# Optimization experiments

Hardware: AMD Instinct MI355X
Metric: run time of the kernel (lower is better)

The kernel has to match this reference:

```python
import jax, jax.numpy as jnp
import numpy as np
from jax import lax

V, D, H, L, NH, OUT = 30000, 300, 512, 2, 8, 3
HD = 2 * H // NH  # 128
B, S = 32, 512


def setup_inputs() -> dict:
    key = jax.random.key(0)
    ks = iter(jax.random.split(key, 64))
    def p(*shape):
        return jax.random.normal(next(ks), shape, jnp.float32) * 0.02
    inp = {"x": jax.random.randint(next(ks), (B, S), 0, V)}
    inp["emb"] = p(V, D)
    for l in range(L):
        isz = D if l == 0 else 2 * H
        for d in ("f", "b"):
            inp[f"Wih_{l}{d}"] = p(4 * H, isz)
            inp[f"Whh_{l}{d}"] = p(4 * H, H)
            inp[f"bih_{l}{d}"] = p(4 * H)
            inp[f"bhh_{l}{d}"] = p(4 * H)
    inp["Wq"], inp["bq"] = p(NH, 2 * H, HD), p(NH, HD)
    inp["Wk"], inp["bk"] = p(NH, 2 * H, HD), p(NH, HD)
    inp["Wv"], inp["bv"] = p(NH, 2 * H, HD), p(NH, HD)
    inp["Wfc"], inp["bfc"] = p(OUT, 2 * H), p(OUT)
    return inp


def _lstm_dir(x, Wih, Whh, bih, bhh, reverse):
    # x: [B,S,I]; PyTorch gate order i,f,g,o
    xg = jnp.einsum('bsi,gi->sbg', x, Wih) + bih  # precomputed input projections [S,B,4H]
    Bn = x.shape[0]
    init = (jnp.zeros((Bn, H), x.dtype), jnp.zeros((Bn, H), x.dtype))
    def step(carry, xt):
        h, c = carry
        g = xt + h @ Whh.T + bhh
        i, f, gg, o = jnp.split(g, 4, axis=-1)
        c = jax.nn.sigmoid(f) * c + jax.nn.sigmoid(i) * jnp.tanh(gg)
        h = jax.nn.sigmoid(o) * jnp.tanh(c)
        return (h, c), h
    _, hs = lax.scan(step, init, xg, reverse=reverse)
    return jnp.swapaxes(hs, 0, 1)  # [B,S,H]


def _forward(x, emb, lstm_params, Wq, bq, Wk, bk, Wv, bv, Wfc, bfc):
    h = emb[x]  # [B,S,D]
    for (Wf, Uf, bf1, bf2, Wb, Ub, bb1, bb2) in lstm_params:
        fwd = _lstm_dir(h, Wf, Uf, bf1, bf2, reverse=False)
        bwd = _lstm_dir(h, Wb, Ub, bb1, bb2, reverse=True)
        h = jnp.concatenate([fwd, bwd], axis=-1)  # [B,S,2H]
    # multi-head attention over LSTM outputs (heads batched instead of python loop)
    Q = jnp.einsum('bsd,hde->bhse', h, Wq) + bq[None, :, None, :]
    K = jnp.einsum('bsd,hde->bhse', h, Wk) + bk[None, :, None, :]
    Vv = jnp.einsum('bsd,hde->bhse', h, Wv) + bv[None, :, None, :]
    scores = jax.nn.softmax(jnp.einsum('bhse,bhte->bhst', Q, K) / np.sqrt(HD).astype(np.float32), axis=-1)
    ctx = jnp.einsum('bhst,bhte->bhse', scores, Vv)
    ctx = jnp.transpose(ctx, (0, 2, 1, 3)).reshape(ctx.shape[0], ctx.shape[2], NH * HD)  # concat heads
    pooled = jnp.mean(ctx, axis=1)  # [B,2H]
    return pooled @ Wfc.T + bfc


def reference(x, emb,
              Wih_0f, Whh_0f, bih_0f, bhh_0f, Wih_0b, Whh_0b, bih_0b, bhh_0b,
              Wih_1f, Whh_1f, bih_1f, bhh_1f, Wih_1b, Whh_1b, bih_1b, bhh_1b,
              Wq, bq, Wk, bk, Wv, bv, Wfc, bfc):
    lstm_params = [
        (Wih_0f, Whh_0f, bih_0f, bhh_0f, Wih_0b, Whh_0b, bih_0b, bhh_0b),
        (Wih_1f, Whh_1f, bih_1f, bhh_1f, Wih_1b, Whh_1b, bih_1b, bhh_1b),
    ]
    return _forward(x, emb, lstm_params, Wq, bq, Wk, bk, Wv, bv, Wfc, bfc)
```

## Files before the change

kernel.cpp:

```cpp
#include <hip/hip_runtime.h>
#include <hip/hip_bf16.h>
#include <math.h>

#define S_LEN 512
#define BATCH 32
#define HID   512
#define G4    2048
#define DIM   300
#define NHEAD 8
#define HDIM  128
#define CH    64
#define NCH   8

typedef __hip_bfloat16 bf16;

#define OFF_XGC   0ull
#define OFF_HCAT0 8388608ull
#define OFF_HCAT1 25165824ull
#define OFF_H0    25165824ull
#define OFF_WP    41943040ull
#define OFF_PB    45088768ull
#define OFF_CT    45091840ull
#define OFF_HT    45124608ull
#define OFF_POOL  45190144ull

__global__ void k_embed(const int* __restrict__ x, const float* __restrict__ emb,
                        float* __restrict__ h0)
{
    int p = blockIdx.x;
    int row = x[p];
    const float* src = emb + (size_t)row * DIM;
    float* dst = h0 + (size_t)p * DIM;
    for (int d = threadIdx.x; d < DIM; d += blockDim.x) dst[d] = src[d];
}

__global__ __launch_bounds__(256) void k_xgc(const float* __restrict__ A, int lda,
    const float* __restrict__ Wf, const float* __restrict__ Wb,
    const float* __restrict__ bihf, const float* __restrict__ bhhf,
    const float* __restrict__ bihb, const float* __restrict__ bhhb,
    float* __restrict__ xgc, int K, int c64)
{
    __shared__ float As[8][128];
    __shared__ float Bs[8][128];
    int tid = threadIdx.x;
    int dir = blockIdx.z;
    int m0 = blockIdx.y * 128, n0 = blockIdx.x * 128;
    const float* W  = dir ? Wb : Wf;
    const float* b1 = dir ? bihb : bihf;
    const float* b2 = dir ? bhhb : bhhf;
    int tx = tid & 15, ty = tid >> 4;

    float acc[8][8];
#pragma unroll
    for (int i = 0; i < 8; i++)
#pragma unroll
        for (int j = 0; j < 8; j++) acc[i][j] = 0.f;

    for (int k0 = 0; k0 < K; k0 += 8) {
#pragma unroll
        for (int e4 = 0; e4 < 4; e4++) {
            int e = tid * 4 + e4;
            int kl = e & 7, ml = e >> 3;
            int kk = k0 + kl;
            int m = m0 + ml;
            int slot = m >> 5, bb = m & 31;
            int s = dir ? (S_LEN - 1 - c64 - slot) : (c64 + slot);
            As[kl][ml] = (kk < K) ? A[((size_t)bb * S_LEN + s) * lda + kk] : 0.f;
            Bs[kl][ml] = (kk < K) ? W[(size_t)(n0 + ml) * K + kk] : 0.f;
        }
        __syncthreads();
#pragma unroll
        for (int k = 0; k < 8; k++) {
            float a[8], b[8];
#pragma unroll
            for (int i = 0; i < 8; i++) a[i] = As[k][ty + 16 * i];
#pragma unroll
            for (int j = 0; j < 8; j++) b[j] = Bs[k][tx + 16 * j];
#pragma unroll
            for (int i = 0; i < 8; i++)
#pragma unroll
                for (int j = 0; j < 8; j++) acc[i][j] += a[i] * b[j];
        }
        __syncthreads();
    }

#pragma unroll
    for (int i = 0; i < 8; i++) {
        int m = m0 + ty + 16 * i;
        int slot = m >> 5, bb = m & 31;
#pragma unroll
        for (int j = 0; j < 8; j++) {
            int n = n0 + tx + 16 * j;
            xgc[(((size_t)dir * CH + slot) * G4 + n) * BATCH + bb] =
                acc[i][j] + b1[n] + b2[n];
        }
    }
}

__global__ __launch_bounds__(256) void k_step(const float* __restrict__ xgc,
    const float* __restrict__ Whh_f, const float* __restrict__ Whh_b,
    float* __restrict__ hT, float* __restrict__ cT, float* __restrict__ hcat, int tt)
{
    int wg = blockIdx.x;
    int dir = wg >> 7, ublk = wg & 127;
    int u0 = ublk * 4;
    const float* Whh = dir ? Whh_b : Whh_f;
    int s_cur = dir ? (S_LEN - 1 - tt) : tt;
    int slot = tt & (CH - 1);
    int tid = threadIdx.x;
    int b  = tid & 31;
    int uu = (tid >> 5) & 3;
    int kh = tid >> 7;
    int u = u0 + uu;

    float acc0 = 0.f, acc1 = 0.f, acc2 = 0.f, acc3 = 0.f;
    if (tt > 0) {
        const float* hTd = hT + ((size_t)((tt & 1) ^ 1) * 2 + dir) * 16384;
        int k0 = kh * 256;
        const float4* w0 = (const float4*)(Whh + ((size_t)(0 * HID + u)) * HID + k0);
        const float4* w1 = (const float4*)(Whh + ((size_t)(1 * HID + u)) * HID + k0);
        const float4* w2 = (const float4*)(Whh + ((size_t)(2 * HID + u)) * HID + k0);
        const float4* w3 = (const float4*)(Whh + ((size_t)(3 * HID + u)) * HID + k0);
        const float* hb = hTd + (size_t)k0 * 32 + b;
#pragma unroll 8
        for (int k4 = 0; k4 < 64; k4++) {
            float h0v = hb[(k4 * 4 + 0) * 32];
            float h1v = hb[(k4 * 4 + 1) * 32];
            float h2v = hb[(k4 * 4 + 2) * 32];
            float h3v = hb[(k4 * 4 + 3) * 32];
            float4 a0 = w0[k4], a1 = w1[k4], a2 = w2[k4], a3 = w3[k4];
            acc0 += a0.x * h0v + a0.y * h1v + a0.z * h2v + a0.w * h3v;
            acc1 += a1.x * h0v + a1.y * h1v + a1.z * h2v + a1.w * h3v;
            acc2 += a2.x * h0v + a2.y * h1v + a2.z * h2v + a2.w * h3v;
            acc3 += a3.x * h0v + a3.y * h1v + a3.z * h2v + a3.w * h3v;
        }
    }

    __shared__ float red[4][4][32];
    if (kh) {
        red[uu][0][b] = acc0; red[uu][1][b] = acc1;
        red[uu][2][b] = acc2; red[uu][3][b] = acc3;
    }
    __syncthreads();
    if (!kh) {
        size_t xbase = (((size_t)dir * CH + slot) * G4) * BATCH;
        float gi = acc0 + red[uu][0][b] + xgc[xbase + (size_t)(0 * HID + u) * BATCH + b];
        float gf = acc1 + red[uu][1][b] + xgc[xbase + (size_t)(1 * HID + u) * BATCH + b];
        float gg = acc2 + red[uu][2][b] + xgc[xbase + (size_t)(2 * HID + u) * BATCH + b];
        float go = acc3 + red[uu][3][b] + xgc[xbase + (size_t)(3 * HID + u) * BATCH + b];
        size_t ci = ((size_t)dir * HID + u) * 32 + b;
        float cp = (tt > 0) ? cT[ci] : 0.f;
        float si = 1.f / (1.f + expf(-gi));
        float sf = 1.f / (1.f + expf(-gf));
        float so = 1.f / (1.f + expf(-go));
        float cn = sf * cp + si * tanhf(gg);
        float hn = so * tanhf(cn);
        cT[ci] = cn;
        hT[((size_t)(tt & 1) * 2 + dir) * 16384 + (size_t)u * 32 + b] = hn;
        hcat[((size_t)b * S_LEN + s_cur) * 1024 + dir * HID + u] = hn;
    }
}

__global__ void k_pack(const float* __restrict__ Wq, const float* __restrict__ Wk,
                       const float* __restrict__ Wv, const float* __restrict__ bq,
                       const float* __restrict__ bk, const float* __restrict__ bv,
                       float* __restrict__ Wp, float* __restrict__ pb)
{
    size_t i = (size_t)blockIdx.x * 256 + threadIdx.x;
    if (i < 3ull * 1024 * 1024) {
        int tt = (int)(i >> 20);
        int w  = (int)(i & 1048575);
        int n  = w >> 10;
        int d  = w & 1023;
        int hh = n >> 7, e = n & 127;
        const float* W = (tt == 0) ? Wq : (tt == 1 ? Wk : Wv);
        Wp[i] = W[((size_t)hh * 1024 + d) * 128 + e];
    }
    if (i < 3072) {
        int tt = (int)(i >> 10), w = (int)(i & 1023);
        const float* bb = (tt == 0) ? bq : (tt == 1 ? bk : bv);
        pb[i] = bb[w];
    }
}

__global__ __launch_bounds__(256) void k_qkv(const float* __restrict__ A,
    const float* __restrict__ Wp, const float* __restrict__ pb,
    bf16* __restrict__ Qout)
{
    __shared__ float As[8][128];
    __shared__ float Bs[8][128];
    int tid = threadIdx.x;
    int m0 = blockIdx.y * 128, n0 = blockIdx.x * 128;
    int tx = tid & 15, ty = tid >> 4;

    float acc[8][8];
#pragma unroll
    for (int i = 0; i < 8; i++)
#pragma unroll
        for (int j = 0; j < 8; j++) acc[i][j] = 0.f;

    for (int k0 = 0; k0 < 1024; k0 += 8) {
#pragma unroll
        for (int e4 = 0; e4 < 4; e4++) {
            int e = tid * 4 + e4;
            int kl = e & 7, ml = e >> 3;
            int kk = k0 + kl;
            As[kl][ml] = A[(size_t)(m0 + ml) * 1024 + kk];
            Bs[kl][ml] = Wp[(size_t)(n0 + ml) * 1024 + kk];
        }
        __syncthreads();
#pragma unroll
        for (int k = 0; k < 8; k++) {
            float a[8], b[8];
#pragma unroll
            for (int i = 0; i < 8; i++) a[i] = As[k][ty + 16 * i];
#pragma unroll
            for (int j = 0; j < 8; j++) b[j] = Bs[k][tx + 16 * j];
#pragma unroll
            for (int i = 0; i < 8; i++)
#pragma unroll
                for (int j = 0; j < 8; j++) acc[i][j] += a[i] * b[j];
        }
        __syncthreads();
    }

#pragma unroll
    for (int i = 0; i < 8; i++) {
        int m = m0 + ty + 16 * i;
        int b = m >> 9, s = m & 511;
#pragma unroll
        for (int j = 0; j < 8; j++) {
            int n = n0 + tx + 16 * j;
            int tt = n >> 10, w = n & 1023, hh = w >> 7, e = w & 127;
            float v = acc[i][j] + pb[n];
            Qout[(size_t)tt * 16777216ull +
                 ((size_t)(b * NHEAD + hh) * S_LEN + s) * HDIM + e] = __float2bfloat16(v);
        }
    }
}

__global__ __launch_bounds__(256) void k_attn(const bf16* __restrict__ Q,
    const bf16* __restrict__ K, const bf16* __restrict__ V,
    float* __restrict__ pooled)
{
    int bh = blockIdx.x;
    int b = bh >> 3, h = bh & 7;
    const bf16* Qb = Q + (size_t)bh * S_LEN * HDIM;
    const bf16* Kb = K + (size_t)bh * S_LEN * HDIM;
    const bf16* Vb = V + (size_t)bh * S_LEN * HDIM;

    __shared__ float Qs[16][HDIM];
    __shared__ float Ss[16][S_LEN + 4];
    __shared__ float wsum[S_LEN];

    int tid = threadIdx.x;
    for (int t = tid; t < S_LEN; t += 256) wsum[t] = 0.f;
    const float SC = 0.08838834764831845f;

    for (int rb = 0; rb < 32; rb++) {
        __syncthreads();
        for (int e = tid; e < 16 * HDIM; e += 256) {
            int rr = e >> 7, ee = e & 127;
            Qs[rr][ee] = __bfloat162float(Qb[(size_t)(rb * 16 + rr) * HDIM + ee]);
        }
        __syncthreads();
        float acc0[16], acc1[16];
#pragma unroll
        for (int r = 0; r < 16; r++) { acc0[r] = 0.f; acc1[r] = 0.f; }
        const bf16* k0p = Kb + (size_t)tid * HDIM;
        const bf16* k1p = Kb + (size_t)(tid + 256) * HDIM;
        for (int k = 0; k < HDIM; k += 4) {
            short4 r0 = *(const short4*)(k0p + k);
            short4 r1 = *(const short4*)(k1p + k);
            float k0x = __bfloat162float(*(const bf16*)&r0.x);
            float k0y = __bfloat162float(*(const bf16*)&r0.y);
            float k0z = __bfloat162float(*(const bf16*)&r0.z);
            float k0w = __bfloat162float(*(const bf16*)&r0.w);
            float k1x = __bfloat162float(*(const bf16*)&r1.x);
            float k1y = __bfloat162float(*(const bf16*)&r1.y);
            float k1z = __bfloat162float(*(const bf16*)&r1.z);
            float k1w = __bfloat162float(*(const bf16*)&r1.w);
#pragma unroll
            for (int r = 0; r < 16; r++) {
                float4 q = *(const float4*)&Qs[r][k];
                acc0[r] += q.x * k0x + q.y * k0y + q.z * k0z + q.w * k0w;
                acc1[r] += q.x * k1x + q.y * k1y + q.z * k1z + q.w * k1w;
            }
        }
#pragma unroll
        for (int r = 0; r < 16; r++) {
            Ss[r][tid] = acc0[r];
            Ss[r][tid + 256] = acc1[r];
        }
        __syncthreads();
        {
            int r = tid >> 4, l = tid & 15;
            float m = -1e30f;
            for (int t = l; t < S_LEN; t += 16) m = fmaxf(m, Ss[r][t]);
#pragma unroll
            for (int o = 1; o < 16; o <<= 1) m = fmaxf(m, __shfl_xor(m, o));
            float sum = 0.f;
            for (int t = l; t < S_LEN; t += 16) {
                float p = expf((Ss[r][t] - m) * SC);
                Ss[r][t] = p;
                sum += p;
            }
#pragma unroll
            for (int o = 1; o < 16; o <<= 1) sum += __shfl_xor(sum, o);
            float inv = 1.f / sum;
            for (int t = l; t < S_LEN; t += 16) Ss[r][t] *= inv;
        }
        __syncthreads();
        for (int t = tid; t < S_LEN; t += 256) {
            float s = 0.f;
#pragma unroll
            for (int rr = 0; rr < 16; rr++) s += Ss[rr][t];
            wsum[t] += s;
        }
    }
    __syncthreads();

    if (tid < HDIM) {
        float a = 0.f;
        for (int t = 0; t < S_LEN; t++)
            a += wsum[t] * __bfloat162float(Vb[(size_t)t * HDIM + tid]);
        pooled[(size_t)b * 1024 + h * HDIM + tid] = a * (1.0f / S_LEN);
    }
}

__global__ void k_fc(const float* __restrict__ pooled, const float* __restrict__ Wfc,
                     const float* __restrict__ bfc, float* __restrict__ out)
{
    int j = threadIdx.x;
    if (j < 96) {
        int b = j / 3, o = j - b * 3;
        float a = bfc[o];
        for (int k = 0; k < 1024; k++)
            a += pooled[(size_t)b * 1024 + k] * Wfc[(size_t)o * 1024 + k];
        out[j] = a;
    }
}

extern "C" void kernel_launch(void* const* d_in, const int* in_sizes, int n_in,
                              void* d_out, int out_size, void* d_ws, size_t ws_size,
                              hipStream_t stream)
{
    const int*   x     = (const int*)d_in[0];
    const float* emb   = (const float*)d_in[1];
    const float* Wih0f = (const float*)d_in[2];
    const float* Whh0f = (const float*)d_in[3];
    const float* bih0f = (const float*)d_in[4];
    const float* bhh0f = (const float*)d_in[5];
    const float* Wih0b = (const float*)d_in[6];
    const float* Whh0b = (const float*)d_in[7];
    const float* bih0b = (const float*)d_in[8];
    const float* bhh0b = (const float*)d_in[9];
    const float* Wih1f = (const float*)d_in[10];
    const float* Whh1f = (const float*)d_in[11];
    const float* bih1f = (const float*)d_in[12];
    const float* bhh1f = (const float*)d_in[13];
    const float* Wih1b = (const float*)d_in[14];
    const float* Whh1b = (const float*)d_in[15];
    const float* bih1b = (const float*)d_in[16];
    const float* bhh1b = (const float*)d_in[17];
    const float* Wq    = (const float*)d_in[18];
    const float* bq    = (const float*)d_in[19];
    const float* Wk    = (const float*)d_in[20];
    const float* bk    = (const float*)d_in[21];
    const float* Wv    = (const float*)d_in[22];
    const float* bv    = (const float*)d_in[23];
    const float* Wfc   = (const float*)d_in[24];
    const float* bfc   = (const float*)d_in[25];

    float* ws     = (float*)d_ws;
    float* xgc    = ws + OFF_XGC;
    float* hcat0  = ws + OFF_HCAT0;
    float* hcat1  = ws + OFF_HCAT1;
    float* h0     = ws + OFF_H0;
    float* Wp     = ws + OFF_WP;
    float* pb     = ws + OFF_PB;
    float* cT     = ws + OFF_CT;
    float* hT     = ws + OFF_HT;
    float* pooled = ws + OFF_POOL;
    bf16*  Qbf    = (bf16*)ws;
    bf16*  Kbf    = Qbf + 16777216ull;
    bf16*  Vbf    = Qbf + 33554432ull;

    dim3 blk(256);

    k_embed<<<BATCH * S_LEN, 128, 0, stream>>>(x, emb, h0);
    k_pack<<<12288, 256, 0, stream>>>(Wq, Wk, Wv, bq, bk, bv, Wp, pb);

    for (int c = 0; c < NCH; c++) {
        k_xgc<<<dim3(16, 16, 2), blk, 0, stream>>>(h0, DIM, Wih0f, Wih0b,
            bih0f, bhh0f, bih0b, bhh0b, xgc, DIM, c * CH);
        for (int i = 0; i < CH; i++)
            k_step<<<256, blk, 0, stream>>>(xgc, Whh0f, Whh0b, hT, cT, hcat0, c * CH + i);
    }
    for (int c = 0; c < NCH; c++) {
        k_xgc<<<dim3(16, 16, 2), blk, 0, stream>>>(hcat0, 1024, Wih1f, Wih1b,
            bih1f, bhh1f, bih1b, bhh1b, xgc, 1024, c * CH);
        for (int i = 0; i < CH; i++)
            k_step<<<256, blk, 0, stream>>>(xgc, Whh1f, Whh1b, hT, cT, hcat1, c * CH + i);
    }

    k_qkv<<<dim3(24, 128), blk, 0, stream>>>(hcat1, Wp, pb, Qbf);
    k_attn<<<256, blk, 0, stream>>>(Qbf, Kbf, Vbf, pooled);
    k_fc<<<1, 128, 0, stream>>>(pooled, Wfc, bfc, (float*)d_out);
}
```

Baseline: 24.19 ms.

## Replace per-timestep LSTM launches with persistent chunk kernel and grid barrier

```diff
diff --git a/kernel.cpp b/kernel.cpp
--- a/kernel.cpp
+++ b/kernel.cpp
@@ -21,8 +21,9 @@
 #define OFF_WP    41943040ull
 #define OFF_PB    45088768ull
 #define OFF_CT    45091840ull
-#define OFF_HT    45124608ull
+#define OFF_HG    45124608ull
 #define OFF_POOL  45190144ull
+#define OFF_BAR   45222912ull
 
 __global__ void k_embed(const int* __restrict__ x, const float* __restrict__ emb,
                         float* __restrict__ h0)
@@ -97,68 +98,119 @@
     }
 }
 
-__global__ __launch_bounds__(256) void k_step(const float* __restrict__ xgc,
+__global__ __launch_bounds__(512) void k_chunk(const float* __restrict__ xgc,
     const float* __restrict__ Whh_f, const float* __restrict__ Whh_b,
-    float* __restrict__ hT, float* __restrict__ cT, float* __restrict__ hcat, int tt)
-{
+    float* __restrict__ hG, float* __restrict__ cT, float* __restrict__ hcat,
+    unsigned int* __restrict__ bar, int c64)
+{
+    __shared__ float Wldsf[16 * 512];
     int wg = blockIdx.x;
     int dir = wg >> 7, ublk = wg & 127;
     int u0 = ublk * 4;
     const float* Whh = dir ? Whh_b : Whh_f;
-    int s_cur = dir ? (S_LEN - 1 - tt) : tt;
-    int slot = tt & (CH - 1);
     int tid = threadIdx.x;
-    int b  = tid & 31;
-    int uu = (tid >> 5) & 3;
-    int kh = tid >> 7;
-    int u = u0 + uu;
-
-    float acc0 = 0.f, acc1 = 0.f, acc2 = 0.f, acc3 = 0.f;
-    if (tt > 0) {
-        const float* hTd = hT + ((size_t)((tt & 1) ^ 1) * 2 + dir) * 16384;
-        int k0 = kh * 256;
-        const float4* w0 = (const float4*)(Whh + ((size_t)(0 * HID + u)) * HID + k0);
-        const float4* w1 = (const float4*)(Whh + ((size_t)(1 * HID + u)) * HID + k0);
-        const float4* w2 = (const float4*)(Whh + ((size_t)(2 * HID + u)) * HID + k0);
-        const float4* w3 = (const float4*)(Whh + ((size_t)(3 * HID + u)) * HID + k0);
-        const float* hb = hTd + (size_t)k0 * 32 + b;
-#pragma unroll 8
-        for (int k4 = 0; k4 < 64; k4++) {
-            float h0v = hb[(k4 * 4 + 0) * 32];
-            float h1v = hb[(k4 * 4 + 1) * 32];
-            float h2v = hb[(k4 * 4 + 2) * 32];
-            float h3v = hb[(k4 * 4 + 3) * 32];
-            float4 a0 = w0[k4], a1 = w1[k4], a2 = w2[k4], a3 = w3[k4];
-            acc0 += a0.x * h0v + a0.y * h1v + a0.z * h2v + a0.w * h3v;
-            acc1 += a1.x * h0v + a1.y * h1v + a1.z * h2v + a1.w * h3v;
-            acc2 += a2.x * h0v + a2.y * h1v + a2.z * h2v + a2.w * h3v;
-            acc3 += a3.x * h0v + a3.y * h1v + a3.z * h2v + a3.w * h3v;
-        }
-    }
-
-    __shared__ float red[4][4][32];
-    if (kh) {
-        red[uu][0][b] = acc0; red[uu][1][b] = acc1;
-        red[uu][2][b] = acc2; red[uu][3][b] = acc3;
+    int ks = tid & 15, b = tid >> 4;
+    int gid = wg & 7;
+
+#pragma unroll
+    for (int j = 0; j < 16; j++) {
+        int idx = tid + 512 * j;
+        int r = idx >> 9, k = idx & 511;
+        int grow = (r >> 2) * HID + u0 + (r & 3);
+        int kp = k ^ (((k >> 5) & 7) << 2);
+        Wldsf[r * 512 + kp] = Whh[(size_t)grow * HID + k];
     }
     __syncthreads();
-    if (!kh) {
-        size_t xbase = (((size_t)dir * CH + slot) * G4) * BATCH;
-        float gi = acc0 + red[uu][0][b] + xgc[xbase + (size_t)(0 * HID + u) * BATCH + b];
-        float gf = acc1 + red[uu][1][b] + xgc[xbase + (size_t)(1 * HID + u) * BATCH + b];
-        float gg = acc2 + red[uu][2][b] + xgc[xbase + (size_t)(2 * HID + u) * BATCH + b];
-        float go = acc3 + red[uu][3][b] + xgc[xbase + (size_t)(3 * HID + u) * BATCH + b];
-        size_t ci = ((size_t)dir * HID + u) * 32 + b;
-        float cp = (tt > 0) ? cT[ci] : 0.f;
-        float si = 1.f / (1.f + expf(-gi));
-        float sf = 1.f / (1.f + expf(-gf));
-        float so = 1.f / (1.f + expf(-go));
-        float cn = sf * cp + si * tanhf(gg);
-        float hn = so * tanhf(cn);
-        cT[ci] = cn;
-        hT[((size_t)(tt & 1) * 2 + dir) * 16384 + (size_t)u * 32 + b] = hn;
-        hcat[((size_t)b * S_LEN + s_cur) * 1024 + dir * HID + u] = hn;
-    }
+
+    const float4* Wl4 = (const float4*)Wldsf;
+    int ks7 = ks & 7;
+
+    float c_reg = 0.f;
+    size_t ci = 0;
+    if (ks < 4) {
+        ci = ((size_t)dir * HID + u0 + ks) * BATCH + b;
+        if (c64 > 0) c_reg = cT[ci];
+    }
+
+    for (int i = 0; i < CH; i++) {
+        int tt = c64 + i;
+        int s_cur = dir ? (S_LEN - 1 - tt) : tt;
+
+        float xv0 = 0.f, xv1 = 0.f, xv2 = 0.f, xv3 = 0.f;
+        if (ks < 4) {
+            size_t xb = (((size_t)dir * CH + i) * G4) * BATCH + b;
+            xv0 = xgc[xb + (size_t)(0 * HID + u0 + ks) * BATCH];
+            xv1 = xgc[xb + (size_t)(1 * HID + u0 + ks) * BATCH];
+            xv2 = xgc[xb + (size_t)(2 * HID + u0 + ks) * BATCH];
+            xv3 = xgc[xb + (size_t)(3 * HID + u0 + ks) * BATCH];
+        }
+
+        float rsum[16];
+#pragma unroll
+        for (int r = 0; r < 16; r++) rsum[r] = 0.f;
+
+        if (tt > 0) {
+            int pr = (tt & 1) ^ 1;
+            const float4* hp =
+                (const float4*)(hG + ((size_t)(pr * 2 + dir) * BATCH + b) * HID) + ks * 8;
+            float4 hh[8];
+#pragma unroll
+            for (int j = 0; j < 8; j++) hh[j] = hp[j];
+#pragma unroll
+            for (int r = 0; r < 16; r++) {
+                float a = 0.f;
+#pragma unroll
+                for (int j = 0; j < 8; j++) {
+                    float4 w = Wl4[r * 128 + ks * 8 + (j ^ ks7)];
+                    a += w.x * hh[j].x + w.y * hh[j].y + w.z * hh[j].z + w.w * hh[j].w;
+                }
+                rsum[r] = a;
+            }
+#pragma unroll
+            for (int m = 1; m < 16; m <<= 1)
+#pragma unroll
+                for (int r = 0; r < 16; r++)
+                    rsum[r] += __shfl_xor(rsum[r], m);
+        }
+
+        if (ks < 4) {
+            int uu = ks;
+            float g0 = 0.f, g1 = 0.f, g2 = 0.f, g3 = 0.f;
+            if (tt > 0) {
+                g0 = uu == 0 ? rsum[0]  : uu == 1 ? rsum[1]  : uu == 2 ? rsum[2]  : rsum[3];
+                g1 = uu == 0 ? rsum[4]  : uu == 1 ? rsum[5]  : uu == 2 ? rsum[6]  : rsum[7];
+                g2 = uu == 0 ? rsum[8]  : uu == 1 ? rsum[9]  : uu == 2 ? rsum[10] : rsum[11];
+                g3 = uu == 0 ? rsum[12] : uu == 1 ? rsum[13] : uu == 2 ? rsum[14] : rsum[15];
+            }
+            g0 += xv0; g1 += xv1; g2 += xv2; g3 += xv3;
+            float si = 1.f / (1.f + expf(-g0));
+            float sf = 1.f / (1.f + expf(-g1));
+            float so = 1.f / (1.f + expf(-g3));
+            float cn = sf * c_reg + si * tanhf(g2);
+            float hn = so * tanhf(cn);
+            c_reg = cn;
+            int pw = tt & 1;
+            hG[((size_t)(pw * 2 + dir) * BATCH + b) * HID + u0 + uu] = hn;
+            hcat[((size_t)b * S_LEN + s_cur) * 1024 + dir * HID + u0 + uu] = hn;
+        }
+
+        __syncthreads();
+        if (tid == 0) {
+            unsigned tgt = (unsigned)(i + 1);
+            unsigned old = __hip_atomic_fetch_add(&bar[32 + gid * 16], 1u,
+                                                  __ATOMIC_ACQ_REL, __HIP_MEMORY_SCOPE_AGENT);
+            if (old == 32u * tgt - 1u) {
+                unsigned r2 = __hip_atomic_fetch_add(&bar[16], 1u,
+                                                     __ATOMIC_ACQ_REL, __HIP_MEMORY_SCOPE_AGENT);
+                if (r2 == 8u * tgt - 1u)
+                    __hip_atomic_store(&bar[0], tgt, __ATOMIC_RELEASE, __HIP_MEMORY_SCOPE_AGENT);
+            }
+            while (__hip_atomic_load(&bar[0], __ATOMIC_ACQUIRE, __HIP_MEMORY_SCOPE_AGENT) < tgt)
+                __builtin_amdgcn_s_sleep(2);
+        }
+        __syncthreads();
+    }
+    if (ks < 4) cT[ci] = c_reg;
 }
 
 __global__ void k_pack(const float* __restrict__ Wq, const float* __restrict__ Wk,
@@ -380,8 +432,9 @@
     float* Wp     = ws + OFF_WP;
     float* pb     = ws + OFF_PB;
     float* cT     = ws + OFF_CT;
-    float* hT     = ws + OFF_HT;
+    float* hG     = ws + OFF_HG;
     float* pooled = ws + OFF_POOL;
+    unsigned int* bar = (unsigned int*)(ws + OFF_BAR);
     bf16*  Qbf    = (bf16*)ws;
     bf16*  Kbf    = Qbf + 16777216ull;
     bf16*  Vbf    = Qbf + 33554432ull;
@@ -394,14 +447,14 @@
     for (int c = 0; c < NCH; c++) {
         k_xgc<<<dim3(16, 16, 2), blk, 0, stream>>>(h0, DIM, Wih0f, Wih0b,
             bih0f, bhh0f, bih0b, bhh0b, xgc, DIM, c * CH);
-        for (int i = 0; i < CH; i++)
-            k_step<<<256, blk, 0, stream>>>(xgc, Whh0f, Whh0b, hT, cT, hcat0, c * CH + i);
+        hipMemsetAsync(bar, 0, 1024, stream);
+        k_chunk<<<256, 512, 0, stream>>>(xgc, Whh0f, Whh0b, hG, cT, hcat0, bar, c * CH);
     }
     for (int c = 0; c < NCH; c++) {
         k_xgc<<<dim3(16, 16, 2), blk, 0, stream>>>(hcat0, 1024, Wih1f, Wih1b,
             bih1f, bhh1f, bih1b, bhh1b, xgc, 1024, c * CH);
-        for (int i = 0; i < CH; i++)
-            k_step<<<256, blk, 0, stream>>>(xgc, Whh1f, Whh1b, hT, cT, hcat1, c * CH + i);
+        hipMemsetAsync(bar, 0, 1024, stream);
+        k_chunk<<<256, 512, 0, stream>>>(xgc, Whh1f, Whh1b, hG, cT, hcat1, bar, c * CH);
     }
 
     k_qkv<<<dim3(24, 128), blk, 0, stream>>>(hcat1, Wp, pb, Qbf);
```

Result: slower. 34.24 ms (+41.6%).
